# Performance work log

Hardware: AMD Instinct MI355X
Metric: run time of the kernel (lower is better)

The kernel has to match this reference:

```python
import jax, jax.numpy as jnp
import numpy as np

D_MODEL = 512
NUM_HEADS = 8
HEAD_DIM = D_MODEL // NUM_HEADS
NUM_ATOM_TYPES = 100
NEG_INF = float('-inf')


def setup_inputs() -> dict:
    key = jax.random.key(0)
    ks = jax.random.split(key, 16)
    B, S, A = 16, 2048, 128
    inp = {
        'protein_repr': jax.random.normal(ks[0], (B, S, D_MODEL), jnp.float32),
        'ligand_repr': jax.random.normal(ks[1], (B, A, D_MODEL), jnp.float32),
        'protein_coords': jax.random.normal(ks[2], (B, S, 3), jnp.float32) * 10.0,
        'ligand_coords': jax.random.normal(ks[3], (B, A, 3), jnp.float32) * 10.0,
        'ligand_atom_types': jax.random.randint(ks[4], (B, A), 0, NUM_ATOM_TYPES, jnp.int64),
        'ligand_mask': jax.random.bernoulli(ks[5], 0.9, (B, A)).at[:, 0].set(True),
    }
    s = 1.0 / np.sqrt(D_MODEL)
    inp['Wq'] = jax.random.normal(ks[6], (D_MODEL, D_MODEL), jnp.float32) * s
    inp['bq'] = jnp.zeros((D_MODEL,), jnp.float32)
    inp['Wk'] = jax.random.normal(ks[7], (D_MODEL, D_MODEL), jnp.float32) * s
    inp['bk'] = jnp.zeros((D_MODEL,), jnp.float32)
    inp['Wv'] = jax.random.normal(ks[8], (D_MODEL, D_MODEL), jnp.float32) * s
    inp['bv'] = jnp.zeros((D_MODEL,), jnp.float32)
    inp['Wo'] = jax.random.normal(ks[9], (D_MODEL, D_MODEL), jnp.float32) * s
    inp['bo'] = jnp.zeros((D_MODEL,), jnp.float32)
    inp['Wd'] = jax.random.normal(ks[10], (1, NUM_HEADS), jnp.float32)  # distance_bias Linear(1, H)
    inp['bd'] = jnp.zeros((NUM_HEADS,), jnp.float32)
    inp['atom_emb'] = jax.random.normal(ks[11], (NUM_ATOM_TYPES, NUM_HEADS), jnp.float32)
    return inp


def reference(protein_repr, ligand_repr, protein_coords, ligand_coords,
              ligand_atom_types, ligand_mask,
              Wq, bq, Wk, bk, Wv, bv, Wo, bo, Wd, bd, atom_emb):
    B, S, _ = protein_repr.shape
    A = ligand_repr.shape[1]
    H, Dh = NUM_HEADS, HEAD_DIM
    scale = np.sqrt(Dh).astype(np.float32)

    q = (protein_repr @ Wq + bq).reshape(B, S, H, Dh)   # [B,S,H,Dh]
    k = (ligand_repr @ Wk + bk).reshape(B, A, H, Dh)    # [B,A,H,Dh]
    v = (ligand_repr @ Wv + bv).reshape(B, A, H, Dh)

    scores = jnp.einsum('bshd,bahd->bhsa', q, k) / scale  # [B,H,S,A]

    # distance bias: pairwise ||p - l|| then Linear(1 -> H)
    diff = protein_coords[:, :, None, :] - ligand_coords[:, None, :, :]  # [B,S,A,3]
    dist = jnp.sqrt(jnp.sum(diff * diff, axis=-1))                        # [B,S,A]
    dist_bias = dist[..., None] * Wd[0] + bd                              # [B,S,A,H]
    scores = scores + jnp.transpose(dist_bias, (0, 3, 1, 2))

    # atom-type embedding bias: [B,A,H] -> broadcast over S
    atom_bias = atom_emb[ligand_atom_types]                               # [B,A,H]
    scores = scores + jnp.transpose(atom_bias, (0, 2, 1))[:, :, None, :]

    # ligand mask
    scores = jnp.where(ligand_mask[:, None, None, :], scores, NEG_INF)

    attn = jax.nn.softmax(scores, axis=-1)                                # [B,H,S,A]
    out = jnp.einsum('bhsa,bahd->bshd', attn, v).reshape(B, S, H * Dh)
    return out @ Wo + bo
```

## Files before the change

kernel.cpp:

```cpp
#include <hip/hip_runtime.h>
#include <hip/hip_bf16.h>


typedef __attribute__((ext_vector_type(8))) short short8;
typedef __attribute__((ext_vector_type(4))) float f32x4;
typedef __attribute__((ext_vector_type(4))) unsigned int u32x4;

#define MFMA16(a, b, c) __builtin_amdgcn_mfma_f32_16x16x32_bf16((a), (b), (c), 0, 0, 0)
#define LOG2E 1.44269504088896340736f

__device__ __forceinline__ unsigned int cvtpk(float lo, float hi) {
  unsigned int r;
  asm("v_cvt_pk_bf16_f32 %0, %1, %2" : "=v"(r) : "v"(lo), "v"(hi));
  return r;
}
__device__ __forceinline__ short f2bf1(float f) {
  return (short)(cvtpk(f, f) & 0xffffu);
}
__device__ __forceinline__ short f2bf(float f) {
  unsigned int u = __float_as_uint(f);
  u += 0x7FFFu + ((u >> 16) & 1u);
  return (short)(u >> 16);
}
__device__ __forceinline__ float bexp2(float x) {
  float r;
  asm("v_exp_f32 %0, %1" : "=v"(r) : "v"(x));
  return r;
}

__global__ __launch_bounds__(256)
void prep_kernel(const float* __restrict__ Wq, const float* __restrict__ Wk,
                 const float* __restrict__ Wv, const float* __restrict__ Wo,
                 unsigned short* __restrict__ dst,
                 const int* __restrict__ types, const int* __restrict__ mask,
                 const float* __restrict__ bd, const float* __restrict__ aemb,
                 float* __restrict__ bav2) {
  if (blockIdx.z == 4) {
    if (blockIdx.y != 0) return;
    int t = blockIdx.x * 256 + threadIdx.x;
    int msk = mask[t];
    int tp = types[t];
    int b = t >> 7, a = t & 127;
#pragma unroll
    for (int h = 0; h < 8; h++)
      bav2[((size_t)b * 8 + h) * 128 + a] =
          msk ? (aemb[tp * 8 + h] + bd[h]) * LOG2E : -1e30f;
    return;
  }
  __shared__ float t[64][65];
  const int wsel = blockIdx.z;
  const float* src = (wsel == 0) ? Wq : (wsel == 1) ? Wk : (wsel == 2) ? Wv : Wo;
  unsigned short* d = dst + (size_t)wsel * 512 * 512;
  const int k0 = blockIdx.x * 64, n0 = blockIdx.y * 64;
  const int c = threadIdx.x & 63, r4 = threadIdx.x >> 6;
#pragma unroll
  for (int i = 0; i < 16; i++) {
    int row = i * 4 + r4;
    t[row][c] = src[(size_t)(k0 + row) * 512 + n0 + c];
  }
  __syncthreads();
#pragma unroll
  for (int i = 0; i < 16; i++) {
    int row = i * 4 + r4;
    d[(size_t)(n0 + row) * 512 + k0 + c] = (unsigned short)f2bf(t[c][row]);
  }
}

__global__ __launch_bounds__(512)
void kvproj_kernel(const float* __restrict__ ligand,
                   const unsigned short* __restrict__ WkT,
                   const unsigned short* __restrict__ WvT,
                   const float* __restrict__ bk, const float* __restrict__ bv,
                   unsigned short* __restrict__ kbuf,
                   unsigned short* __restrict__ vtbuf) {
  __shared__ short st[128 * 64];
  char* sb = (char*)st;
  const int kv = blockIdx.x, b = blockIdx.y;
  const unsigned short* WT = kv ? WvT : WkT;
  const float* bias = kv ? bv : bk;
  const int tid = threadIdx.x, lane = tid & 63, w = tid >> 6;
  const int c = lane & 15, g = lane >> 4;
  const f32x4 fz = {0.f, 0.f, 0.f, 0.f};
  f32x4 acc[8][4];
#pragma unroll
  for (int i = 0; i < 8; i++)
#pragma unroll
    for (int j = 0; j < 4; j++) acc[i][j] = fz;
  const int srow = tid >> 2, sq = tid & 3;
  for (int kb = 0; kb < 8; kb++) {
    const float* src = ligand + ((size_t)(b * 128 + srow) * 512 + kb * 64 + sq * 16);
    float4 x0 = ((const float4*)src)[0];
    float4 x1 = ((const float4*)src)[1];
    float4 x2 = ((const float4*)src)[2];
    float4 x3 = ((const float4*)src)[3];
    short8 v0, v1;
    v0[0] = f2bf(x0.x); v0[1] = f2bf(x0.y); v0[2] = f2bf(x0.z); v0[3] = f2bf(x0.w);
    v0[4] = f2bf(x1.x); v0[5] = f2bf(x1.y); v0[6] = f2bf(x1.z); v0[7] = f2bf(x1.w);
    v1[0] = f2bf(x2.x); v1[1] = f2bf(x2.y); v1[2] = f2bf(x2.z); v1[3] = f2bf(x2.w);
    v1[4] = f2bf(x3.x); v1[5] = f2bf(x3.y); v1[6] = f2bf(x3.z); v1[7] = f2bf(x3.w);
    *(short8*)(sb + srow * 128 + ((sq * 32) ^ ((srow & 7) << 4))) = v0;
    *(short8*)(sb + srow * 128 + ((sq * 32 + 16) ^ ((srow & 7) << 4))) = v1;
    __syncthreads();
#pragma unroll
    for (int kk = 0; kk < 64; kk += 32) {
      short8 af[8];
#pragma unroll
      for (int mt = 0; mt < 8; mt++) {
        int row = mt * 16 + c;
        af[mt] = *(const short8*)(sb + row * 128 + ((kk * 2 + g * 16) ^ ((row & 7) << 4)));
      }
#pragma unroll
      for (int nt = 0; nt < 4; nt++) {
        short8 bf = *(const short8*)(WT + (size_t)(w * 64 + nt * 16 + c) * 512 +
                                     kb * 64 + kk + g * 8);
#pragma unroll
        for (int mt = 0; mt < 8; mt++)
          acc[mt][nt] = MFMA16(af[mt], bf, acc[mt][nt]);
      }
    }
    __syncthreads();
  }
#pragma unroll
  for (int nt = 0; nt < 4; nt++) {
    int col = w * 64 + nt * 16 + c;
    float bs = bias[col];
    int h = col >> 6, dd = col & 63;
#pragma unroll
    for (int mt = 0; mt < 8; mt++)
#pragma unroll
      for (int r = 0; r < 4; r++) {
        int a = mt * 16 + g * 4 + r;
        unsigned short us = (unsigned short)f2bf(acc[mt][nt][r] + bs);
        if (!kv) {
          kbuf[((size_t)(b * 8 + h) * 128 + a) * 64 + dd] = us;
        } else {
          int pos = (mt >> 1) * 32 + g * 8 + (mt & 1) * 4 + r;
          vtbuf[((size_t)(b * 8 + h) * 64 + dd) * 128 + pos] = us;
        }
      }
  }
}

__global__ __launch_bounds__(512, 2)
void fused_kernel(const float* __restrict__ protein, const float* __restrict__ pcoord,
                  const float* __restrict__ lcoord, const float* __restrict__ Wdp,
                  const float* __restrict__ bq, const float* __restrict__ bo,
                  const unsigned short* __restrict__ WqT,
                  const unsigned short* __restrict__ WoT,
                  const unsigned short* __restrict__ kbuf,
                  const unsigned short* __restrict__ vtbuf,
                  const float* __restrict__ bav2, float* __restrict__ out) {
  __shared__ short8 qao_v[4096];
  __shared__ __align__(16) float distl[8192];
  char* qb = (char*)qao_v;

  const int b = blockIdx.y, s0 = blockIdx.x * 64;
  const int tid = threadIdx.x, lane = tid & 63, w = tid >> 6;
  const int c = lane & 15, g = lane >> 4;
  const f32x4 fz = {0.f, 0.f, 0.f, 0.f};

#pragma unroll
  for (int i = 0; i < 8; i++) {
    int idx = i * 512 + tid;
    const float* src = protein + (size_t)(b * 2048 + s0) * 512 + idx * 8;
    float4 x0 = ((const float4*)src)[0];
    float4 x1 = ((const float4*)src)[1];
    uint4 v;
    v.x = cvtpk(x0.x, x0.y); v.y = cvtpk(x0.z, x0.w);
    v.z = cvtpk(x1.x, x1.y); v.w = cvtpk(x1.z, x1.w);
    int row = idx >> 6, sl = idx & 63;
    *(uint4*)(qb + row * 1024 + ((sl * 16) ^ ((row & 7) << 4))) = v;
  }
  {
    int s = tid >> 3, a0 = (tid & 7) * 16;
    const float* p3 = pcoord + (size_t)(b * 2048 + s0 + s) * 3;
    float px = p3[0], py = p3[1], pz = p3[2];
#pragma unroll
    for (int ii = 0; ii < 4; ii++) {
      f32x4 d4;
#pragma unroll
      for (int r = 0; r < 4; r++) {
        int a = a0 + ii * 4 + r;
        const float* l3 = lcoord + (size_t)(b * 128 + a) * 3;
        float dx = px - l3[0], dy = py - l3[1], dz = pz - l3[2];
        d4[r] = sqrtf(dx * dx + dy * dy + dz * dz);
      }
      *(f32x4*)(distl + s * 128 + ((a0 + ii * 4) ^ ((s & 7) << 2))) = d4;
    }
  }
  __syncthreads();

  f32x4 accq[4][4];
#pragma unroll
  for (int i = 0; i < 4; i++)
#pragma unroll
    for (int j = 0; j < 4; j++) accq[i][j] = fz;
  for (int kp = 0; kp < 16; kp++) {
    short8 bfr[4], afr[4];
#pragma unroll
    for (int nt = 0; nt < 4; nt++)
      bfr[nt] = *(const short8*)(WqT + (size_t)(w * 64 + nt * 16 + c) * 512 +
                                 kp * 32 + g * 8);
#pragma unroll
    for (int mt = 0; mt < 4; mt++) {
      int row = mt * 16 + c;
      afr[mt] = *(const short8*)(qb + row * 1024 +
                                 ((kp * 64 + g * 16) ^ ((row & 7) << 4)));
    }
#pragma unroll
    for (int nt = 0; nt < 4; nt++)
#pragma unroll
      for (int mt = 0; mt < 4; mt++)
        accq[mt][nt] = MFMA16(afr[mt], bfr[nt], accq[mt][nt]);
  }
  __syncthreads();

#pragma unroll
  for (int nt = 0; nt < 4; nt++) {
    int n = w * 64 + nt * 16 + c;
    float bqv = bq[n];
    int chunk = w * 2 + (nt >> 1);
    int p = (nt & 1) * 16 + c;
#pragma unroll
    for (int mt = 0; mt < 4; mt++)
#pragma unroll
      for (int r = 0; r < 4; r++) {
        int s = mt * 16 + g * 4 + r;
        int slot = p ^ (((s & 1) << 3) | (((s >> 2) & 1) << 4));
        *(short*)(qb + (chunk * 64 + s) * 64 + slot * 2) =
            f2bf1(accq[mt][nt][r] + bqv);
      }
  }

  const int h = w;
  const float wdh2 = Wdp[h] * LOG2E;
  const float c1 = 0.125f * LOG2E;
  const unsigned short* kb_h = kbuf + (size_t)(b * 8 + h) * 128 * 64;
  const unsigned short* vt_h = vtbuf + (size_t)(b * 8 + h) * 64 * 128;
  const float* bav_h = bav2 + (size_t)(b * 8 + h) * 128;

  short8 qf[4][2];
#pragma unroll
  for (int st = 0; st < 4; st++) {
    int s = st * 16 + c;
    int sx = ((s & 1) << 3) | (((s >> 2) & 1) << 4);
#pragma unroll
    for (int kq = 0; kq < 2; kq++)
      qf[st][kq] = *(const short8*)(qb + ((h * 2 + kq) * 64 + s) * 64 +
                                    ((g * 8) ^ sx) * 2);
  }
  f32x4 sc[8][4];
#pragma unroll
  for (int i = 0; i < 8; i++)
#pragma unroll
    for (int j = 0; j < 4; j++) sc[i][j] = fz;
#pragma unroll
  for (int at = 0; at < 8; at++) {
    const unsigned short* kr = kb_h + (at * 16 + c) * 64;
    short8 kf0 = *(const short8*)(kr + g * 8);
    short8 kf1 = *(const short8*)(kr + 32 + g * 8);
#pragma unroll
    for (int st = 0; st < 4; st++) sc[at][st] = MFMA16(kf0, qf[st][0], sc[at][st]);
#pragma unroll
    for (int st = 0; st < 4; st++) sc[at][st] = MFMA16(kf1, qf[st][1], sc[at][st]);
  }
  float mx[4] = {-3e38f, -3e38f, -3e38f, -3e38f};
#pragma unroll
  for (int at = 0; at < 8; at++) {
    f32x4 bv = *(const f32x4*)(bav_h + at * 16 + g * 4);
#pragma unroll
    for (int st = 0; st < 4; st++) {
      int s = st * 16 + c;
      f32x4 dd = *(const f32x4*)(distl + s * 128 +
                                 ((at * 16 + g * 4) ^ ((s & 7) << 2)));
#pragma unroll
      for (int r = 0; r < 4; r++) {
        float v = fmaf(sc[at][st][r], c1, fmaf(dd[r], wdh2, bv[r]));
        sc[at][st][r] = v;
        mx[st] = fmaxf(mx[st], v);
      }
    }
  }
#pragma unroll
  for (int st = 0; st < 4; st++) {
    mx[st] = fmaxf(mx[st], __shfl_xor(mx[st], 16));
    mx[st] = fmaxf(mx[st], __shfl_xor(mx[st], 32));
  }
  float sum[4] = {0.f, 0.f, 0.f, 0.f};
#pragma unroll
  for (int at = 0; at < 8; at++)
#pragma unroll
    for (int st = 0; st < 4; st++)
#pragma unroll
      for (int r = 0; r < 4; r++) {
        float p = bexp2(sc[at][st][r] - mx[st]);
        sc[at][st][r] = p;
        sum[st] += p;
      }
#pragma unroll
  for (int st = 0; st < 4; st++) {
    sum[st] += __shfl_xor(sum[st], 16);
    sum[st] += __shfl_xor(sum[st], 32);
  }
  float rinv[4];
#pragma unroll
  for (int st = 0; st < 4; st++) rinv[st] = 1.f / sum[st];

  f32x4 pv[4][4];
#pragma unroll
  for (int i = 0; i < 4; i++)
#pragma unroll
    for (int j = 0; j < 4; j++) pv[i][j] = fz;
#pragma unroll
  for (int ch = 0; ch < 4; ch++) {
    short8 pf[4];
#pragma unroll
    for (int st = 0; st < 4; st++) {
      u32x4 up;
      up[0] = cvtpk(sc[2 * ch][st][0], sc[2 * ch][st][1]);
      up[1] = cvtpk(sc[2 * ch][st][2], sc[2 * ch][st][3]);
      up[2] = cvtpk(sc[2 * ch + 1][st][0], sc[2 * ch + 1][st][1]);
      up[3] = cvtpk(sc[2 * ch + 1][st][2], sc[2 * ch + 1][st][3]);
      pf[st] = __builtin_bit_cast(short8, up);
    }
#pragma unroll
    for (int dt = 0; dt < 4; dt++) {
      short8 vf = *(const short8*)(vt_h + (dt * 16 + c) * 128 + ch * 32 + g * 8);
#pragma unroll
      for (int st = 0; st < 4; st++) pv[dt][st] = MFMA16(vf, pf[st], pv[dt][st]);
    }
  }
#pragma unroll
  for (int dt = 0; dt < 4; dt++) {
    int chunk = h * 2 + (dt >> 1);
    int pbase = (dt & 1) * 16 + g * 4;
#pragma unroll
    for (int st = 0; st < 4; st++) {
      int s = st * 16 + c;
      int sx = ((s & 1) << 3) | (((s >> 2) & 1) << 4);
      uint2 wv;
      wv.x = cvtpk(pv[dt][st][0] * rinv[st], pv[dt][st][1] * rinv[st]);
      wv.y = cvtpk(pv[dt][st][2] * rinv[st], pv[dt][st][3] * rinv[st]);
      *(uint2*)(qb + (chunk * 64 + s) * 64 + (pbase ^ sx) * 2) = wv;
    }
  }
  __syncthreads();

  f32x4 acco[4][4];
#pragma unroll
  for (int i = 0; i < 4; i++)
#pragma unroll
    for (int j = 0; j < 4; j++) acco[i][j] = fz;
  for (int kc = 0; kc < 16; kc++) {
    short8 af[4], bf[4];
#pragma unroll
    for (int nt = 0; nt < 4; nt++)
      af[nt] = *(const short8*)(WoT + (size_t)(w * 64 + nt * 16 + c) * 512 +
                                kc * 32 + g * 8);
#pragma unroll
    for (int st = 0; st < 4; st++) {
      int s = st * 16 + c;
      int sx = ((s & 1) << 3) | (((s >> 2) & 1) << 4);
      bf[st] = *(const short8*)(qb + (kc * 64 + s) * 64 + ((g * 8) ^ sx) * 2);
    }
#pragma unroll
    for (int nt = 0; nt < 4; nt++)
#pragma unroll
      for (int st = 0; st < 4; st++)
        acco[nt][st] = MFMA16(af[nt], bf[st], acco[nt][st]);
  }
#pragma unroll
  for (int nt = 0; nt < 4; nt++) {
    f32x4 bo4 = *(const f32x4*)(bo + w * 64 + nt * 16 + g * 4);
#pragma unroll
    for (int st = 0; st < 4; st++) {
      int s = st * 16 + c;
      f32x4 o;
#pragma unroll
      for (int r = 0; r < 4; r++) o[r] = acco[nt][st][r] + bo4[r];
      *(f32x4*)(out + (size_t)(b * 2048 + s0 + s) * 512 + w * 64 + nt * 16 + g * 4) = o;
    }
  }
}

extern "C" void kernel_launch(void* const* d_in, const int* in_sizes, int n_in,
                              void* d_out, int out_size, void* d_ws, size_t ws_size,
                              hipStream_t stream) {
  const float* protein = (const float*)d_in[0];
  const float* ligand  = (const float*)d_in[1];
  const float* pcoord  = (const float*)d_in[2];
  const float* lcoord  = (const float*)d_in[3];
  const int*   atypes  = (const int*)d_in[4];
  const int*   lmask   = (const int*)d_in[5];
  const float* Wq = (const float*)d_in[6];
  const float* bq = (const float*)d_in[7];
  const float* Wk = (const float*)d_in[8];
  const float* bk = (const float*)d_in[9];
  const float* Wv = (const float*)d_in[10];
  const float* bv = (const float*)d_in[11];
  const float* Wo = (const float*)d_in[12];
  const float* bo = (const float*)d_in[13];
  const float* Wd = (const float*)d_in[14];
  const float* bd = (const float*)d_in[15];
  const float* aemb = (const float*)d_in[16];

  char* ws = (char*)d_ws;
  const size_t WSLOT = (size_t)512 * 512 * 2;
  unsigned short* WqT = (unsigned short*)(ws + 0 * WSLOT);
  unsigned short* WkT = (unsigned short*)(ws + 1 * WSLOT);
  unsigned short* WvT = (unsigned short*)(ws + 2 * WSLOT);
  unsigned short* WoT = (unsigned short*)(ws + 3 * WSLOT);
  unsigned short* kbuf  = (unsigned short*)(ws + 4 * WSLOT);
  unsigned short* vtbuf = (unsigned short*)(ws + 4 * WSLOT + (2u << 20));
  float* bav2 = (float*)(ws + 4 * WSLOT + (4u << 20));

  prep_kernel<<<dim3(8, 8, 5), 256, 0, stream>>>(Wq, Wk, Wv, Wo, WqT,
                                                 atypes, lmask, bd, aemb, bav2);
  kvproj_kernel<<<dim3(2, 16), 512, 0, stream>>>(ligand, WkT, WvT, bk, bv, kbuf, vtbuf);
  fused_kernel<<<dim3(32, 16), 512, 0, stream>>>(protein, pcoord, lcoord, Wd, bq, bo,
                                                 WqT, WoT, kbuf, vtbuf, bav2,
                                                 (float*)d_out);
}
```

Before: 290.1 us.

## Shrink fused tiles to 32 rows, store distances as fp16, split KV projection

The fused attention kernel now handles 32 protein rows per block with 256 threads (4 waves, 2 heads each), so more blocks can be resident and the grid doubles. The distance table is packed as fp16 to cut LDS use, and the LDS layout for Q and attention output is reorganised around per-head 128-byte rows. The KV projection grid is split four ways over output columns for more parallelism, and the prep kernel is flattened to a 1D grid with fewer wasted blocks. Each block now reloads the full Wq and Wo for half as many rows, and fp16 distances lose some precision.

```diff
diff --git a/kernel.cpp b/kernel.cpp
--- a/kernel.cpp
+++ b/kernel.cpp
@@ -13,6 +13,16 @@
   unsigned int r;
   asm("v_cvt_pk_bf16_f32 %0, %1, %2" : "=v"(r) : "v"(lo), "v"(hi));
   return r;
+}
+__device__ __forceinline__ unsigned int pkf16(float lo, float hi) {
+  unsigned int r;
+  asm("v_cvt_pkrtz_f16_f32 %0, %1, %2" : "=v"(r) : "v"(lo), "v"(hi));
+  return r;
+}
+__device__ __forceinline__ float f16f(unsigned short u) {
+  _Float16 h;
+  __builtin_memcpy(&h, &u, 2);
+  return (float)h;
 }
 __device__ __forceinline__ short f2bf1(float f) {
   return (short)(cvtpk(f, f) & 0xffffu);
@@ -35,23 +45,26 @@
                  const int* __restrict__ types, const int* __restrict__ mask,
                  const float* __restrict__ bd, const float* __restrict__ aemb,
                  float* __restrict__ bav2) {
-  if (blockIdx.z == 4) {
-    if (blockIdx.y != 0) return;
-    int t = blockIdx.x * 256 + threadIdx.x;
-    int msk = mask[t];
-    int tp = types[t];
-    int b = t >> 7, a = t & 127;
-#pragma unroll
-    for (int h = 0; h < 8; h++)
-      bav2[((size_t)b * 8 + h) * 128 + a] =
-          msk ? (aemb[tp * 8 + h] + bd[h]) * LOG2E : -1e30f;
+  const int bid = blockIdx.x;
+  if (bid == 256) {
+#pragma unroll
+    for (int it = 0; it < 8; it++) {
+      int t = it * 256 + threadIdx.x;
+      int msk = mask[t];
+      int tp = types[t];
+      int b = t >> 7, a = t & 127;
+#pragma unroll
+      for (int h = 0; h < 8; h++)
+        bav2[((size_t)b * 8 + h) * 128 + a] =
+            msk ? (aemb[tp * 8 + h] + bd[h]) * LOG2E : -1e30f;
+    }
     return;
   }
   __shared__ float t[64][65];
-  const int wsel = blockIdx.z;
+  const int wsel = bid >> 6, tile = bid & 63;
   const float* src = (wsel == 0) ? Wq : (wsel == 1) ? Wk : (wsel == 2) ? Wv : Wo;
   unsigned short* d = dst + (size_t)wsel * 512 * 512;
-  const int k0 = blockIdx.x * 64, n0 = blockIdx.y * 64;
+  const int k0 = (tile >> 3) * 64, n0 = (tile & 7) * 64;
   const int c = threadIdx.x & 63, r4 = threadIdx.x >> 6;
 #pragma unroll
   for (int i = 0; i < 16; i++) {
@@ -75,17 +88,16 @@
                    unsigned short* __restrict__ vtbuf) {
   __shared__ short st[128 * 64];
   char* sb = (char*)st;
-  const int kv = blockIdx.x, b = blockIdx.y;
+  const int kv = blockIdx.x, b = blockIdx.y, nh = blockIdx.z;
   const unsigned short* WT = kv ? WvT : WkT;
   const float* bias = kv ? bv : bk;
   const int tid = threadIdx.x, lane = tid & 63, w = tid >> 6;
   const int c = lane & 15, g = lane >> 4;
+  const int col = nh * 128 + w * 16 + c;
   const f32x4 fz = {0.f, 0.f, 0.f, 0.f};
-  f32x4 acc[8][4];
-#pragma unroll
-  for (int i = 0; i < 8; i++)
-#pragma unroll
-    for (int j = 0; j < 4; j++) acc[i][j] = fz;
+  f32x4 acc[8];
+#pragma unroll
+  for (int i = 0; i < 8; i++) acc[i] = fz;
   const int srow = tid >> 2, sq = tid & 3;
   for (int kb = 0; kb < 8; kb++) {
     const float* src = ligand + ((size_t)(b * 128 + srow) * 512 + kb * 64 + sq * 16);
@@ -93,36 +105,27 @@
     float4 x1 = ((const float4*)src)[1];
     float4 x2 = ((const float4*)src)[2];
     float4 x3 = ((const float4*)src)[3];
-    short8 v0, v1;
-    v0[0] = f2bf(x0.x); v0[1] = f2bf(x0.y); v0[2] = f2bf(x0.z); v0[3] = f2bf(x0.w);
-    v0[4] = f2bf(x1.x); v0[5] = f2bf(x1.y); v0[6] = f2bf(x1.z); v0[7] = f2bf(x1.w);
-    v1[0] = f2bf(x2.x); v1[1] = f2bf(x2.y); v1[2] = f2bf(x2.z); v1[3] = f2bf(x2.w);
-    v1[4] = f2bf(x3.x); v1[5] = f2bf(x3.y); v1[6] = f2bf(x3.z); v1[7] = f2bf(x3.w);
-    *(short8*)(sb + srow * 128 + ((sq * 32) ^ ((srow & 7) << 4))) = v0;
-    *(short8*)(sb + srow * 128 + ((sq * 32 + 16) ^ ((srow & 7) << 4))) = v1;
+    uint4 v0, v1;
+    v0.x = cvtpk(x0.x, x0.y); v0.y = cvtpk(x0.z, x0.w);
+    v0.z = cvtpk(x1.x, x1.y); v0.w = cvtpk(x1.z, x1.w);
+    v1.x = cvtpk(x2.x, x2.y); v1.y = cvtpk(x2.z, x2.w);
+    v1.z = cvtpk(x3.x, x3.y); v1.w = cvtpk(x3.z, x3.w);
+    *(uint4*)(sb + srow * 128 + ((sq * 32) ^ ((srow & 7) << 4))) = v0;
+    *(uint4*)(sb + srow * 128 + ((sq * 32 + 16) ^ ((srow & 7) << 4))) = v1;
     __syncthreads();
 #pragma unroll
     for (int kk = 0; kk < 64; kk += 32) {
-      short8 af[8];
+      short8 bf = *(const short8*)(WT + (size_t)col * 512 + kb * 64 + kk + g * 8);
 #pragma unroll
       for (int mt = 0; mt < 8; mt++) {
         int row = mt * 16 + c;
-        af[mt] = *(const short8*)(sb + row * 128 + ((kk * 2 + g * 16) ^ ((row & 7) << 4)));
-      }
-#pragma unroll
-      for (int nt = 0; nt < 4; nt++) {
-        short8 bf = *(const short8*)(WT + (size_t)(w * 64 + nt * 16 + c) * 512 +
-                                     kb * 64 + kk + g * 8);
-#pragma unroll
-        for (int mt = 0; mt < 8; mt++)
-          acc[mt][nt] = MFMA16(af[mt], bf, acc[mt][nt]);
+        short8 af = *(const short8*)(sb + row * 128 + ((kk * 2 + g * 16) ^ ((row & 7) << 4)));
+        acc[mt] = MFMA16(af, bf, acc[mt]);
       }
     }
     __syncthreads();
   }
-#pragma unroll
-  for (int nt = 0; nt < 4; nt++) {
-    int col = w * 64 + nt * 16 + c;
+  {
     float bs = bias[col];
     int h = col >> 6, dd = col & 63;
 #pragma unroll
@@ -130,7 +133,7 @@
 #pragma unroll
       for (int r = 0; r < 4; r++) {
         int a = mt * 16 + g * 4 + r;
-        unsigned short us = (unsigned short)f2bf(acc[mt][nt][r] + bs);
+        unsigned short us = (unsigned short)f2bf(acc[mt][r] + bs);
         if (!kv) {
           kbuf[((size_t)(b * 8 + h) * 128 + a) * 64 + dd] = us;
         } else {
@@ -141,7 +144,7 @@
   }
 }
 
-__global__ __launch_bounds__(512, 2)
+__global__ __launch_bounds__(256, 4)
 void fused_kernel(const float* __restrict__ protein, const float* __restrict__ pcoord,
                   const float* __restrict__ lcoord, const float* __restrict__ Wdp,
                   const float* __restrict__ bq, const float* __restrict__ bo,
@@ -150,235 +153,243 @@
                   const unsigned short* __restrict__ kbuf,
                   const unsigned short* __restrict__ vtbuf,
                   const float* __restrict__ bav2, float* __restrict__ out) {
-  __shared__ short8 qao_v[4096];
-  __shared__ __align__(16) float distl[8192];
+  __shared__ short8 qao_v[2048];
+  __shared__ __align__(16) unsigned int distl[2048];
   char* qb = (char*)qao_v;
-
-  const int b = blockIdx.y, s0 = blockIdx.x * 64;
+  char* db = (char*)distl;
+
+  const int b = blockIdx.y, s0 = blockIdx.x * 32;
   const int tid = threadIdx.x, lane = tid & 63, w = tid >> 6;
   const int c = lane & 15, g = lane >> 4;
   const f32x4 fz = {0.f, 0.f, 0.f, 0.f};
 
 #pragma unroll
   for (int i = 0; i < 8; i++) {
-    int idx = i * 512 + tid;
+    int idx = i * 256 + tid;
     const float* src = protein + (size_t)(b * 2048 + s0) * 512 + idx * 8;
     float4 x0 = ((const float4*)src)[0];
     float4 x1 = ((const float4*)src)[1];
     uint4 v;
     v.x = cvtpk(x0.x, x0.y); v.y = cvtpk(x0.z, x0.w);
     v.z = cvtpk(x1.x, x1.y); v.w = cvtpk(x1.z, x1.w);
-    int row = idx >> 6, sl = idx & 63;
-    *(uint4*)(qb + row * 1024 + ((sl * 16) ^ ((row & 7) << 4))) = v;
+    int row = idx >> 6, gran = idx & 63;
+    *(uint4*)(qb + row * 1024 + ((gran * 16) ^ ((row & 7) << 4))) = v;
   }
   {
-    int s = tid >> 3, a0 = (tid & 7) * 16;
+    int s = tid >> 3, t7 = tid & 7;
     const float* p3 = pcoord + (size_t)(b * 2048 + s0 + s) * 3;
     float px = p3[0], py = p3[1], pz = p3[2];
 #pragma unroll
-    for (int ii = 0; ii < 4; ii++) {
-      f32x4 d4;
-#pragma unroll
-      for (int r = 0; r < 4; r++) {
-        int a = a0 + ii * 4 + r;
-        const float* l3 = lcoord + (size_t)(b * 128 + a) * 3;
-        float dx = px - l3[0], dy = py - l3[1], dz = pz - l3[2];
-        d4[r] = sqrtf(dx * dx + dy * dy + dz * dz);
-      }
-      *(f32x4*)(distl + s * 128 + ((a0 + ii * 4) ^ ((s & 7) << 2))) = d4;
+    for (int ii = 0; ii < 2; ii++) {
+      uint4 dv;
+#pragma unroll
+      for (int jj = 0; jj < 4; jj++) {
+        float dpair[2];
+#pragma unroll
+        for (int e = 0; e < 2; e++) {
+          int a = t7 * 16 + ii * 8 + jj * 2 + e;
+          const float* l3 = lcoord + (size_t)(b * 128 + a) * 3;
+          float dx = px - l3[0], dy = py - l3[1], dz = pz - l3[2];
+          dpair[e] = sqrtf(dx * dx + dy * dy + dz * dz);
+        }
+        ((unsigned int*)&dv)[jj] = pkf16(dpair[0], dpair[1]);
+      }
+      *(uint4*)(db + s * 256 + ((t7 * 32 + ii * 16) ^ ((s & 7) << 4))) = dv;
     }
   }
   __syncthreads();
 
-  f32x4 accq[4][4];
-#pragma unroll
-  for (int i = 0; i < 4; i++)
-#pragma unroll
-    for (int j = 0; j < 4; j++) accq[i][j] = fz;
+  f32x4 accq[2][8];
+#pragma unroll
+  for (int i = 0; i < 2; i++)
+#pragma unroll
+    for (int j = 0; j < 8; j++) accq[i][j] = fz;
   for (int kp = 0; kp < 16; kp++) {
-    short8 bfr[4], afr[4];
-#pragma unroll
-    for (int nt = 0; nt < 4; nt++)
-      bfr[nt] = *(const short8*)(WqT + (size_t)(w * 64 + nt * 16 + c) * 512 +
+    short8 bfr[8], afr[2];
+#pragma unroll
+    for (int nt = 0; nt < 8; nt++)
+      bfr[nt] = *(const short8*)(WqT + (size_t)(w * 128 + nt * 16 + c) * 512 +
                                  kp * 32 + g * 8);
 #pragma unroll
-    for (int mt = 0; mt < 4; mt++) {
+    for (int mt = 0; mt < 2; mt++) {
       int row = mt * 16 + c;
       afr[mt] = *(const short8*)(qb + row * 1024 +
                                  ((kp * 64 + g * 16) ^ ((row & 7) << 4)));
     }
 #pragma unroll
-    for (int nt = 0; nt < 4; nt++)
-#pragma unroll
-      for (int mt = 0; mt < 4; mt++)
+    for (int nt = 0; nt < 8; nt++)
+#pragma unroll
+      for (int mt = 0; mt < 2; mt++)
         accq[mt][nt] = MFMA16(afr[mt], bfr[nt], accq[mt][nt]);
   }
   __syncthreads();
 
 #pragma unroll
-  for (int nt = 0; nt < 4; nt++) {
-    int n = w * 64 + nt * 16 + c;
+  for (int nt = 0; nt < 8; nt++) {
+    int n = w * 128 + nt * 16 + c;
     float bqv = bq[n];
-    int chunk = w * 2 + (nt >> 1);
-    int p = (nt & 1) * 16 + c;
-#pragma unroll
-    for (int mt = 0; mt < 4; mt++)
+    int chunk = n >> 6, sl = n & 63;
+#pragma unroll
+    for (int mt = 0; mt < 2; mt++)
 #pragma unroll
       for (int r = 0; r < 4; r++) {
         int s = mt * 16 + g * 4 + r;
-        int slot = p ^ (((s & 1) << 3) | (((s >> 2) & 1) << 4));
-        *(short*)(qb + (chunk * 64 + s) * 64 + slot * 2) =
+        *(short*)(qb + chunk * 4096 + s * 128 + ((sl * 2) ^ ((s & 7) << 4))) =
             f2bf1(accq[mt][nt][r] + bqv);
       }
   }
 
-  const int h = w;
-  const float wdh2 = Wdp[h] * LOG2E;
   const float c1 = 0.125f * LOG2E;
-  const unsigned short* kb_h = kbuf + (size_t)(b * 8 + h) * 128 * 64;
-  const unsigned short* vt_h = vtbuf + (size_t)(b * 8 + h) * 64 * 128;
-  const float* bav_h = bav2 + (size_t)(b * 8 + h) * 128;
-
-  short8 qf[4][2];
-#pragma unroll
-  for (int st = 0; st < 4; st++) {
-    int s = st * 16 + c;
-    int sx = ((s & 1) << 3) | (((s >> 2) & 1) << 4);
-#pragma unroll
-    for (int kq = 0; kq < 2; kq++)
-      qf[st][kq] = *(const short8*)(qb + ((h * 2 + kq) * 64 + s) * 64 +
-                                    ((g * 8) ^ sx) * 2);
-  }
-  f32x4 sc[8][4];
+  for (int hh = 0; hh < 2; hh++) {
+    const int h = w * 2 + hh;
+    const float wdh2 = Wdp[h] * LOG2E;
+    const unsigned short* kb_h = kbuf + (size_t)(b * 8 + h) * 128 * 64;
+    const unsigned short* vt_h = vtbuf + (size_t)(b * 8 + h) * 64 * 128;
+    const float* bav_h = bav2 + (size_t)(b * 8 + h) * 128;
+
+    short8 qf[2][2];
+#pragma unroll
+    for (int st = 0; st < 2; st++) {
+      int s = st * 16 + c;
+#pragma unroll
+      for (int kq = 0; kq < 2; kq++)
+        qf[st][kq] = *(const short8*)(qb + h * 4096 + s * 128 +
+                                      ((kq * 64 + g * 16) ^ ((s & 7) << 4)));
+    }
+    f32x4 sc[8][2];
+#pragma unroll
+    for (int i = 0; i < 8; i++)
+#pragma unroll
+      for (int j = 0; j < 2; j++) sc[i][j] = fz;
+#pragma unroll
+    for (int at = 0; at < 8; at++) {
+      const unsigned short* kr = kb_h + (at * 16 + c) * 64;
+      short8 kf0 = *(const short8*)(kr + g * 8);
+      short8 kf1 = *(const short8*)(kr + 32 + g * 8);
+#pragma unroll
+      for (int st = 0; st < 2; st++) sc[at][st] = MFMA16(kf0, qf[st][0], sc[at][st]);
+#pragma unroll
+      for (int st = 0; st < 2; st++) sc[at][st] = MFMA16(kf1, qf[st][1], sc[at][st]);
+    }
+    float mx[2] = {-3e38f, -3e38f};
+#pragma unroll
+    for (int at = 0; at < 8; at++) {
+      f32x4 bv = *(const f32x4*)(bav_h + at * 16 + g * 4);
+#pragma unroll
+      for (int st = 0; st < 2; st++) {
+        int s = st * 16 + c;
+        uint2 du = *(const uint2*)(db + s * 256 +
+                                   (((at * 32 + (g & 2) * 8)) ^ ((s & 7) << 4)) +
+                                   (g & 1) * 8);
+        float d0 = f16f((unsigned short)(du.x & 0xffff));
+        float d1 = f16f((unsigned short)(du.x >> 16));
+        float d2 = f16f((unsigned short)(du.y & 0xffff));
+        float d3 = f16f((unsigned short)(du.y >> 16));
+        f32x4 dd = {d0, d1, d2, d3};
+#pragma unroll
+        for (int r = 0; r < 4; r++) {
+          float v = fmaf(sc[at][st][r], c1, fmaf(dd[r], wdh2, bv[r]));
+          sc[at][st][r] = v;
+          mx[st] = fmaxf(mx[st], v);
+        }
+      }
+    }
+#pragma unroll
+    for (int st = 0; st < 2; st++) {
+      mx[st] = fmaxf(mx[st], __shfl_xor(mx[st], 16));
+      mx[st] = fmaxf(mx[st], __shfl_xor(mx[st], 32));
+    }
+    float sum[2] = {0.f, 0.f};
+#pragma unroll
+    for (int at = 0; at < 8; at++)
+#pragma unroll
+      for (int st = 0; st < 2; st++)
+#pragma unroll
+        for (int r = 0; r < 4; r++) {
+          float p = bexp2(sc[at][st][r] - mx[st]);
+          sc[at][st][r] = p;
+          sum[st] += p;
+        }
+#pragma unroll
+    for (int st = 0; st < 2; st++) {
+      sum[st] += __shfl_xor(sum[st], 16);
+      sum[st] += __shfl_xor(sum[st], 32);
+    }
+    float rinv[2];
+#pragma unroll
+    for (int st = 0; st < 2; st++) rinv[st] = 1.f / sum[st];
+
+    f32x4 pv[4][2];
+#pragma unroll
+    for (int i = 0; i < 4; i++)
+#pragma unroll
+      for (int j = 0; j < 2; j++) pv[i][j] = fz;
+#pragma unroll
+    for (int ch = 0; ch < 4; ch++) {
+      short8 pf[2];
+#pragma unroll
+      for (int st = 0; st < 2; st++) {
+        u32x4 up;
+        up[0] = cvtpk(sc[2 * ch][st][0], sc[2 * ch][st][1]);
+        up[1] = cvtpk(sc[2 * ch][st][2], sc[2 * ch][st][3]);
+        up[2] = cvtpk(sc[2 * ch + 1][st][0], sc[2 * ch + 1][st][1]);
+        up[3] = cvtpk(sc[2 * ch + 1][st][2], sc[2 * ch + 1][st][3]);
+        pf[st] = __builtin_bit_cast(short8, up);
+      }
+#pragma unroll
+      for (int dt = 0; dt < 4; dt++) {
+        short8 vf = *(const short8*)(vt_h + (dt * 16 + c) * 128 + ch * 32 + g * 8);
+#pragma unroll
+        for (int st = 0; st < 2; st++) pv[dt][st] = MFMA16(vf, pf[st], pv[dt][st]);
+      }
+    }
+#pragma unroll
+    for (int dt = 0; dt < 4; dt++) {
+#pragma unroll
+      for (int st = 0; st < 2; st++) {
+        int s = st * 16 + c;
+        uint2 wv;
+        wv.x = cvtpk(pv[dt][st][0] * rinv[st], pv[dt][st][1] * rinv[st]);
+        wv.y = cvtpk(pv[dt][st][2] * rinv[st], pv[dt][st][3] * rinv[st]);
+        *(uint2*)(qb + h * 4096 + s * 128 + (((dt * 32 + g * 8)) ^ ((s & 7) << 4))) = wv;
+      }
+    }
+  }
+  __syncthreads();
+
+  f32x4 acco[8][2];
 #pragma unroll
   for (int i = 0; i < 8; i++)
 #pragma unroll
-    for (int j = 0; j < 4; j++) sc[i][j] = fz;
-#pragma unroll
-  for (int at = 0; at < 8; at++) {
-    const unsigned short* kr = kb_h + (at * 16 + c) * 64;
-    short8 kf0 = *(const short8*)(kr + g * 8);
-    short8 kf1 = *(const short8*)(kr + 32 + g * 8);
-#pragma unroll
-    for (int st = 0; st < 4; st++) sc[at][st] = MFMA16(kf0, qf[st][0], sc[at][st]);
-#pragma unroll
-    for (int st = 0; st < 4; st++) sc[at][st] = MFMA16(kf1, qf[st][1], sc[at][st]);
-  }
-  float mx[4] = {-3e38f, -3e38f, -3e38f, -3e38f};
-#pragma unroll
-  for (int at = 0; at < 8; at++) {
-    f32x4 bv = *(const f32x4*)(bav_h + at * 16 + g * 4);
-#pragma unroll
-    for (int st = 0; st < 4; st++) {
+    for (int j = 0; j < 2; j++) acco[i][j] = fz;
+  for (int kc = 0; kc < 16; kc++) {
+    short8 af[8], bf[2];
+#pragma unroll
+    for (int nt = 0; nt < 8; nt++)
+      af[nt] = *(const short8*)(WoT + (size_t)(w * 128 + nt * 16 + c) * 512 +
+                                kc * 32 + g * 8);
+#pragma unroll
+    for (int st = 0; st < 2; st++) {
       int s = st * 16 + c;
-      f32x4 dd = *(const f32x4*)(distl + s * 128 +
-                                 ((at * 16 + g * 4) ^ ((s & 7) << 2)));
-#pragma unroll
-      for (int r = 0; r < 4; r++) {
-        float v = fmaf(sc[at][st][r], c1, fmaf(dd[r], wdh2, bv[r]));
-        sc[at][st][r] = v;
-        mx[st] = fmaxf(mx[st], v);
-      }
-    }
-  }
-#pragma unroll
-  for (int st = 0; st < 4; st++) {
-    mx[st] = fmaxf(mx[st], __shfl_xor(mx[st], 16));
-    mx[st] = fmaxf(mx[st], __shfl_xor(mx[st], 32));
-  }
-  float sum[4] = {0.f, 0.f, 0.f, 0.f};
-#pragma unroll
-  for (int at = 0; at < 8; at++)
-#pragma unroll
-    for (int st = 0; st < 4; st++)
-#pragma unroll
-      for (int r = 0; r < 4; r++) {
-        float p = bexp2(sc[at][st][r] - mx[st]);
-        sc[at][st][r] = p;
-        sum[st] += p;
-      }
-#pragma unroll
-  for (int st = 0; st < 4; st++) {
-    sum[st] += __shfl_xor(sum[st], 16);
-    sum[st] += __shfl_xor(sum[st], 32);
-  }
-  float rinv[4];
-#pragma unroll
-  for (int st = 0; st < 4; st++) rinv[st] = 1.f / sum[st];
-
-  f32x4 pv[4][4];
-#pragma unroll
-  for (int i = 0; i < 4; i++)
-#pragma unroll
-    for (int j = 0; j < 4; j++) pv[i][j] = fz;
-#pragma unroll
-  for (int ch = 0; ch < 4; ch++) {
-    short8 pf[4];
-#pragma unroll
-    for (int st = 0; st < 4; st++) {
-      u32x4 up;
-      up[0] = cvtpk(sc[2 * ch][st][0], sc[2 * ch][st][1]);
-      up[1] = cvtpk(sc[2 * ch][st][2], sc[2 * ch][st][3]);
-      up[2] = cvtpk(sc[2 * ch + 1][st][0], sc[2 * ch + 1][st][1]);
-      up[3] = cvtpk(sc[2 * ch + 1][st][2], sc[2 * ch + 1][st][3]);
-      pf[st] = __builtin_bit_cast(short8, up);
-    }
-#pragma unroll
-    for (int dt = 0; dt < 4; dt++) {
-      short8 vf = *(const short8*)(vt_h + (dt * 16 + c) * 128 + ch * 32 + g * 8);
-#pragma unroll
-      for (int st = 0; st < 4; st++) pv[dt][st] = MFMA16(vf, pf[st], pv[dt][st]);
-    }
-  }
-#pragma unroll
-  for (int dt = 0; dt < 4; dt++) {
-    int chunk = h * 2 + (dt >> 1);
-    int pbase = (dt & 1) * 16 + g * 4;
-#pragma unroll
-    for (int st = 0; st < 4; st++) {
-      int s = st * 16 + c;
-      int sx = ((s & 1) << 3) | (((s >> 2) & 1) << 4);
-      uint2 wv;
-      wv.x = cvtpk(pv[dt][st][0] * rinv[st], pv[dt][st][1] * rinv[st]);
-      wv.y = cvtpk(pv[dt][st][2] * rinv[st], pv[dt][st][3] * rinv[st]);
-      *(uint2*)(qb + (chunk * 64 + s) * 64 + (pbase ^ sx) * 2) = wv;
-    }
-  }
-  __syncthreads();
-
-  f32x4 acco[4][4];
-#pragma unroll
-  for (int i = 0; i < 4; i++)
-#pragma unroll
-    for (int j = 0; j < 4; j++) acco[i][j] = fz;
-  for (int kc = 0; kc < 16; kc++) {
-    short8 af[4], bf[4];
-#pragma unroll
-    for (int nt = 0; nt < 4; nt++)
-      af[nt] = *(const short8*)(WoT + (size_t)(w * 64 + nt * 16 + c) * 512 +
-                                kc * 32 + g * 8);
-#pragma unroll
-    for (int st = 0; st < 4; st++) {
-      int s = st * 16 + c;
-      int sx = ((s & 1) << 3) | (((s >> 2) & 1) << 4);
-      bf[st] = *(const short8*)(qb + (kc * 64 + s) * 64 + ((g * 8) ^ sx) * 2);
-    }
-#pragma unroll
-    for (int nt = 0; nt < 4; nt++)
-#pragma unroll
-      for (int st = 0; st < 4; st++)
+      bf[st] = *(const short8*)(qb + (kc >> 1) * 4096 + s * 128 +
+                                (((kc & 1) * 64 + g * 16) ^ ((s & 7) << 4)));
+    }
+#pragma unroll
+    for (int nt = 0; nt < 8; nt++)
+#pragma unroll
+      for (int st = 0; st < 2; st++)
         acco[nt][st] = MFMA16(af[nt], bf[st], acco[nt][st]);
   }
 #pragma unroll
-  for (int nt = 0; nt < 4; nt++) {
-    f32x4 bo4 = *(const f32x4*)(bo + w * 64 + nt * 16 + g * 4);
-#pragma unroll
-    for (int st = 0; st < 4; st++) {
+  for (int nt = 0; nt < 8; nt++) {
+    f32x4 bo4 = *(const f32x4*)(bo + w * 128 + nt * 16 + g * 4);
+#pragma unroll
+    for (int st = 0; st < 2; st++) {
       int s = st * 16 + c;
       f32x4 o;
 #pragma unroll
       for (int r = 0; r < 4; r++) o[r] = acco[nt][st][r] + bo4[r];
-      *(f32x4*)(out + (size_t)(b * 2048 + s0 + s) * 512 + w * 64 + nt * 16 + g * 4) = o;
+      *(f32x4*)(out + (size_t)(b * 2048 + s0 + s) * 512 + w * 128 + nt * 16 + g * 4) = o;
     }
   }
 }
@@ -414,10 +425,11 @@
   unsigned short* vtbuf = (unsigned short*)(ws + 4 * WSLOT + (2u << 20));
   float* bav2 = (float*)(ws + 4 * WSLOT + (4u << 20));
 
-  prep_kernel<<<dim3(8, 8, 5), 256, 0, stream>>>(Wq, Wk, Wv, Wo, WqT,
-                                                 atypes, lmask, bd, aemb, bav2);
-  kvproj_kernel<<<dim3(2, 16), 512, 0, stream>>>(ligand, WkT, WvT, bk, bv, kbuf, vtbuf);
-  fused_kernel<<<dim3(32, 16), 512, 0, stream>>>(protein, pcoord, lcoord, Wd, bq, bo,
+  prep_kernel<<<257, 256, 0, stream>>>(Wq, Wk, Wv, Wo, WqT,
+                                       atypes, lmask, bd, aemb, bav2);
+  kvproj_kernel<<<dim3(2, 16, 4), 512, 0, stream>>>(ligand, WkT, WvT, bk, bv,
+                                                    kbuf, vtbuf);
+  fused_kernel<<<dim3(64, 16), 256, 0, stream>>>(protein, pcoord, lcoord, Wd, bq, bo,
                                                  WqT, WoT, kbuf, vtbuf, bav2,
                                                  (float*)d_out);
 }
```

After: 389.2 us. 1.34x slower.
